# Kernel tuning notes

Measured on AMD Instinct MI355X. Metric: run time of the kernel, lower is better.

Reference implementation:

```python
import jax, jax.numpy as jnp
import numpy as np

N_NODES = 50000
N_EDGES = 800000
IN_FEATS = 128
OUT_CLASSES = 128


def _glorot(key, shape):
    fan_in, fan_out = shape[1], shape[0]
    limit = float(np.sqrt(6.0 / (fan_in + fan_out)))
    return jax.random.uniform(key, shape, jnp.float32, -limit, limit)


def setup_inputs() -> dict:
    key = jax.random.key(0)
    ks = jax.random.split(key, 11)
    x = jax.random.normal(ks[0], (N_NODES, IN_FEATS), jnp.float32)
    edge_index = jax.random.randint(ks[1], (2, N_EDGES), 0, N_NODES, jnp.int64)
    h = OUT_CLASSES // 2
    # PyG SAGEConv: lin_l applied to aggregated neighbors (has bias), lin_r to root (no bias)
    return {
        "x": x,
        "edge_index": edge_index,
        "W_l1": _glorot(ks[2], (OUT_CLASSES, IN_FEATS)),
        "b1": jnp.zeros((OUT_CLASSES,), jnp.float32),
        "W_r1": _glorot(ks[3], (OUT_CLASSES, IN_FEATS)),
        "W_l2": _glorot(ks[4], (h, OUT_CLASSES)),
        "b2": jnp.zeros((h,), jnp.float32),
        "W_r2": _glorot(ks[5], (h, OUT_CLASSES)),
        "W_l3": _glorot(ks[6], (OUT_CLASSES, h)),
        "b3": jnp.zeros((OUT_CLASSES,), jnp.float32),
        "W_r3": _glorot(ks[7], (OUT_CLASSES, h)),
    }


def _sage_conv(x, src, dst, W_l, b, W_r):
    # gather source-node features, mean-aggregate at destinations
    msgs = x[src]                                               # [E, d]
    agg = jax.ops.segment_sum(msgs, dst, num_segments=N_NODES)  # [N, d]
    cnt = jax.ops.segment_sum(jnp.ones((src.shape[0], 1), x.dtype), dst,
                              num_segments=N_NODES)             # [N, 1]
    mean = agg / jnp.maximum(cnt, 1.0)
    return mean @ W_l.T + b + x @ W_r.T


def reference(x, edge_index, W_l1, b1, W_r1, W_l2, b2, W_r2, W_l3, b3, W_r3):
    src, dst = edge_index[0], edge_index[1]
    h = _sage_conv(x, src, dst, W_l1, b1, W_r1)
    h = _sage_conv(h, src, dst, W_l2, b2, W_r2)
    h = _sage_conv(h, src, dst, W_l3, b3, W_r3)
    return h
```

## Files before the change

### kernel.cpp

```cpp
#include <hip/hip_runtime.h>

#define N_NODES 50000
#define N_EDGES 800000
#define BUCKETS 196
#define ECHUNK 4096
#define EBLKS 196
#define BCAP 5120

typedef __attribute__((ext_vector_type(8))) _Float16 half8;
typedef __attribute__((ext_vector_type(4))) float f32x4;


template <int L, int DEPTH>
__device__ __forceinline__ void gather_sum(const half8* __restrict__ ip,
                                           const unsigned short* __restrict__ csr,
                                           int start, int d, int lane,
                                           float acc[8]) {
  if (d <= 0) return;
  int nb = (d + DEPTH - 1) / DEPTH;
  int sc[DEPTH];
#pragma unroll
  for (int j = 0; j < DEPTH; ++j) sc[j] = csr[start + (j < d ? j : d - 1)];
  half8 vlast;
  for (int b = 0; b < nb; ++b) {
    half8 v[DEPTH];
#pragma unroll
    for (int j = 0; j < DEPTH; ++j) v[j] = ip[(size_t)sc[j] * L + lane];
    int e2 = (b + 1) * DEPTH;
    if (e2 < d) {
#pragma unroll
      for (int j = 0; j < DEPTH; ++j) {
        int idx = e2 + j;
        sc[j] = csr[start + (idx < d ? idx : d - 1)];
      }
    }
#pragma unroll
    for (int j = 0; j < DEPTH; ++j)
#pragma unroll
      for (int q = 0; q < 8; ++q) acc[q] += (float)v[j][q];
    vlast = v[DEPTH - 1];
  }
  int rem = d - (nb - 1) * DEPTH;
  if (rem < DEPTH) {
    float corr = (float)(DEPTH - rem);
#pragma unroll
    for (int q = 0; q < 8; ++q) acc[q] -= corr * (float)vlast[q];
  }
}


__global__ __launch_bounds__(256) void prep_k(
    const int* __restrict__ src, const int* __restrict__ dst,
    int* __restrict__ gcur, unsigned* __restrict__ binned,
    const float* __restrict__ x, _Float16* __restrict__ xh,
    const float* __restrict__ Wl1, const float* __restrict__ Wr1,
    const float* __restrict__ Wl2, const float* __restrict__ Wr2,
    const float* __restrict__ Wl3, const float* __restrict__ Wr3,
    _Float16* ph_l1, _Float16* pl_l1, _Float16* ph_r1, _Float16* pl_r1,
    _Float16* ph_c2, _Float16* pl_c2, _Float16* ph_l3, _Float16* pl_l3,
    _Float16* ph_r3, _Float16* pl_r3) {
  int blk = blockIdx.x;
  int t = threadIdx.x;
  if (blk < EBLKS) {
    __shared__ int h[BUCKETS];
    __shared__ int base[BUCKETS];
    for (int i = t; i < BUCKETS; i += 256) h[i] = 0;
    __syncthreads();
    int e0 = blk * ECHUNK;
    int eend = e0 + ECHUNK < N_EDGES ? e0 + ECHUNK : N_EDGES;
    for (int e = e0 + t; e < eend; e += 256) atomicAdd(&h[dst[e] >> 8], 1);
    __syncthreads();
    for (int i = t; i < BUCKETS; i += 256) {
      if (h[i]) base[i] = atomicAdd(&gcur[i], h[i]);
      h[i] = 0;
    }
    __syncthreads();
    for (int e = e0 + t; e < eend; e += 256) {
      int d = dst[e];
      int b = d >> 8;
      int r = atomicAdd(&h[b], 1);
      binned[(size_t)b * BCAP + base[b] + r] =
          (unsigned)src[e] | ((unsigned)(d & 255) << 16);
    }
  } else if (blk < EBLKS + 32) {
    int g = (blk - EBLKS) * 256 + t;
    const float *S0, *S1 = nullptr;
    _Float16 *ph, *pl;
    int f, K;
    if (g < 2048)      { f = g;        ph = ph_l1; pl = pl_l1; S0 = Wl1; K = 128; }
    else if (g < 4096) { f = g - 2048; ph = ph_r1; pl = pl_r1; S0 = Wr1; K = 128; }
    else if (g < 6144) { f = g - 4096; ph = ph_c2; pl = pl_c2; S0 = Wl2; S1 = Wr2; K = 128; }
    else if (g < 7168) { f = g - 6144; ph = ph_l3; pl = pl_l3; S0 = Wl3; K = 64; }
    else               { f = g - 7168; ph = ph_r3; pl = pl_r3; S0 = Wr3; K = 64; }
    int kb = f >> 9;
    int rem = f & 511;
    int n = rem >> 2;
    int lq = rem & 3;
    const float* srow =
        (S1 && n >= 64) ? (S1 + (size_t)(n - 64) * K) : (S0 + (size_t)n * K);
    int kbase = kb * 32 + lq * 8;
#pragma unroll
    for (int j = 0; j < 8; ++j) {
      float v = srow[kbase + j];
      _Float16 hi = (_Float16)v;
      ph[f * 8 + j] = hi;
      pl[f * 8 + j] = (_Float16)(v - (float)hi);
    }
  } else {
    int i = (blk - EBLKS - 32) * 256 + t;
    if (i >= N_NODES * 16) return;
    const float4* xp = (const float4*)x;
    float4 a = xp[2 * i];
    float4 b = xp[2 * i + 1];
    half8 hh;
    hh[0] = (_Float16)a.x; hh[1] = (_Float16)a.y; hh[2] = (_Float16)a.z; hh[3] = (_Float16)a.w;
    hh[4] = (_Float16)b.x; hh[5] = (_Float16)b.y; hh[6] = (_Float16)b.z; hh[7] = (_Float16)b.w;
    ((half8*)xh)[i] = hh;
  }
}

__global__ __launch_bounds__(256) void bucket_fill_k(const unsigned* __restrict__ binned,
                                                     const int* __restrict__ gcnt,
                                                     int* __restrict__ offs,
                                                     int* __restrict__ deg,
                                                     unsigned short* __restrict__ csr) {
  __shared__ int cnt[256];
  __shared__ int loc[256];
  __shared__ int cur[256];
  int b = blockIdx.x;
  int t = threadIdx.x;
  int base = b * BCAP;
  int end = base + gcnt[b];
  cnt[t] = 0;
  __syncthreads();
  for (int e = base + t; e < end; e += 256) atomicAdd(&cnt[(binned[e] >> 16) & 255], 1);
  __syncthreads();
  loc[t] = cnt[t];
  __syncthreads();
  for (int o = 1; o < 256; o <<= 1) {
    int v = (t >= o) ? loc[t - o] : 0;
    __syncthreads();
    loc[t] += v;
    __syncthreads();
  }
  int excl = loc[t] - cnt[t];
  int node = b * 256 + t;
  if (node < N_NODES) {
    offs[node] = base + excl;
    deg[node] = cnt[t];
  }
  cur[t] = excl;
  __syncthreads();
  for (int e = base + t; e < end; e += 256) {
    unsigned r = binned[e];
    int dl = (r >> 16) & 255;
    int p = atomicAdd(&cur[dl], 1);
    csr[base + p] = (unsigned short)(r & 0xFFFF);
  }
}


template <int D, bool FUSE>
__global__ __launch_bounds__(256, 4) void agg_f16_k(const _Float16* __restrict__ in,
                                                    _Float16* __restrict__ out,
                                                    const int* __restrict__ offs,
                                                    const int* __restrict__ deg,
                                                    const unsigned short* __restrict__ csr,
                                                    const float* __restrict__ bias,
                                                    const _Float16* __restrict__ addend) {
  constexpr int L = D / 8;
  constexpr int NPB = 256 / L;
  int node = blockIdx.x * NPB + threadIdx.x / L;
  int lane = threadIdx.x & (L - 1);
  if (node >= N_NODES) return;
  int start = offs[node];
  int d = deg[node];
  const half8* ip = (const half8*)in;
  float acc[8];
#pragma unroll
  for (int j = 0; j < 8; ++j) acc[j] = 0.f;
  gather_sum<L, 16>(ip, csr, start, d, lane, acc);
  float inv = d > 0 ? 1.0f / (float)d : 0.0f;
  half8 o;
  if constexpr (FUSE) {
    half8 av = ((const half8*)addend)[(size_t)node * L + lane];
#pragma unroll
    for (int q = 0; q < 8; ++q)
      o[q] = (_Float16)(acc[q] * inv + bias[lane * 8 + q] + (float)av[q]);
  } else {
#pragma unroll
    for (int q = 0; q < 8; ++q) o[q] = (_Float16)(acc[q] * inv);
  }
  ((half8*)out)[(size_t)node * L + lane] = o;
}


template <int K, int NB, bool OUT32>
__global__ __launch_bounds__(256, 4) void fused_agg_gemm_k(
    const _Float16* __restrict__ feat,
    const int* __restrict__ offs, const int* __restrict__ deg,
    const unsigned short* __restrict__ csr,
    const _Float16* __restrict__ Wlh, const _Float16* __restrict__ Wll,
    const _Float16* __restrict__ Wrh, const _Float16* __restrict__ Wrl,
    const float* __restrict__ bias, _Float16* __restrict__ C16,
    float* __restrict__ C32) {
  constexpr int L = K / 8;
  static_assert(256 / L == NB, "one lane-group per node");
  constexpr int STRIDE = K + 8;
  constexpr int KB = K / 32;
  constexpr int ROWG = NB / 16;
  constexpr int WPR = 4 / ROWG;
  constexpr int CT = 8 / WPR;
  __shared__ _Float16 Asm[NB * STRIDE];
  int t = threadIdx.x;
  int base = blockIdx.x * NB;
  const half8* ip = (const half8*)feat;
  {
    int lane = t & (L - 1);
    int slot = t / L;
    int node = base + slot;
    float acc[8];
#pragma unroll
    for (int j = 0; j < 8; ++j) acc[j] = 0.f;
    float inv = 0.f;
    if (node < N_NODES) {
      int start = offs[node];
      int d = deg[node];
      gather_sum<L, 16>(ip, csr, start, d, lane, acc);
      inv = d > 0 ? 1.0f / (float)d : 0.0f;
    }
    half8 o;
#pragma unroll
    for (int q = 0; q < 8; ++q) o[q] = (_Float16)(acc[q] * inv);
    *(half8*)&Asm[slot * STRIDE + lane * 8] = o;
  }
  __syncthreads();
  int wave = t >> 6;
  int lane = t & 63;
  int l15 = lane & 15;
  int lq = lane >> 4;
  int rowg = wave / WPR;
  int colbase = (wave % WPR) * (CT * 16);
  int row0 = base + rowg * 16;
  const int woff = (l15 * 4 + lq) * 8;
  f32x4 acc[CT];
#pragma unroll
  for (int c = 0; c < CT; ++c) acc[c] = (f32x4){0.f, 0.f, 0.f, 0.f};
  {
    const _Float16* asrc = &Asm[(rowg * 16 + l15) * STRIDE + lq * 8];
    half8 af[KB];
#pragma unroll
    for (int kb = 0; kb < KB; ++kb) af[kb] = *(const half8*)(asrc + kb * 32);
#pragma unroll
    for (int kb = 0; kb < KB; ++kb) {
#pragma unroll
      for (int ct = 0; ct < CT; ++ct) {
        size_t bi = (size_t)(kb * 128 + colbase + ct * 16) * 32 + woff;
        half8 bh = *(const half8*)(Wlh + bi);
        half8 bl = *(const half8*)(Wll + bi);
        acc[ct] = __builtin_amdgcn_mfma_f32_16x16x32_f16(af[kb], bh, acc[ct], 0, 0, 0);
        acc[ct] = __builtin_amdgcn_mfma_f32_16x16x32_f16(af[kb], bl, acc[ct], 0, 0, 0);
      }
    }
  }
  {
    int arow = row0 + l15;
    if (arow >= N_NODES) arow = N_NODES - 1;
    const _Float16* ab = feat + (size_t)arow * K + lq * 8;
    half8 af[KB];
#pragma unroll
    for (int kb = 0; kb < KB; ++kb) af[kb] = *(const half8*)(ab + kb * 32);
#pragma unroll
    for (int kb = 0; kb < KB; ++kb) {
#pragma unroll
      for (int ct = 0; ct < CT; ++ct) {
        size_t bi = (size_t)(kb * 128 + colbase + ct * 16) * 32 + woff;
        half8 bh = *(const half8*)(Wrh + bi);
        half8 bl = *(const half8*)(Wrl + bi);
        acc[ct] = __builtin_amdgcn_mfma_f32_16x16x32_f16(af[kb], bh, acc[ct], 0, 0, 0);
        acc[ct] = __builtin_amdgcn_mfma_f32_16x16x32_f16(af[kb], bl, acc[ct], 0, 0, 0);
      }
    }
  }
#pragma unroll
  for (int r = 0; r < 4; ++r) {
    int row = row0 + lq * 4 + r;
    if (row >= N_NODES) continue;
#pragma unroll
    for (int ct = 0; ct < CT; ++ct) {
      int col = colbase + ct * 16 + l15;
      float v = acc[ct][r] + bias[col];
      if constexpr (OUT32)
        C32[(size_t)row * 128 + col] = v;
      else
        C16[(size_t)row * 128 + col] = (_Float16)v;
    }
  }
}


template <int K, bool DUAL, bool SPLIT, bool OUT32>
__global__ __launch_bounds__(256, 2) void gemm_f16_k(
    const _Float16* __restrict__ A1, const _Float16* __restrict__ W1h,
    const _Float16* __restrict__ W1l,
    const _Float16* __restrict__ A2, const _Float16* __restrict__ W2h,
    const _Float16* __restrict__ W2l,
    const float* __restrict__ bias, _Float16* __restrict__ C16,
    float* __restrict__ C32, _Float16* __restrict__ O2) {
  int wave = threadIdx.x >> 6;
  int lane = threadIdx.x & 63;
  int l15 = lane & 15;
  int lq = lane >> 4;
  int rowblk = blockIdx.x >> 1;
  int colg = blockIdx.x & 1;
  int rg = rowblk * 4 + wave;
  if (rg >= N_NODES / 16) return;
  int row0 = rg << 4;
  constexpr int KB = K / 32;
  constexpr int NN = 128;
  const int woff = (l15 * 4 + lq) * 8;
  f32x4 acc[4];
#pragma unroll
  for (int c = 0; c < 4; ++c) acc[c] = (f32x4){0.f, 0.f, 0.f, 0.f};
  constexpr int NOP = DUAL ? 2 : 1;
#pragma unroll
  for (int op = 0; op < NOP; ++op) {
    const _Float16* A = op ? A2 : A1;
    const _Float16* Wh = op ? W2h : W1h;
    const _Float16* Wl = op ? W2l : W1l;
    const _Float16* ab = A + (size_t)(row0 + l15) * K + lq * 8;
    half8 af[KB];
#pragma unroll
    for (int kb = 0; kb < KB; ++kb) af[kb] = *(const half8*)(ab + kb * 32);
#pragma unroll
    for (int kb = 0; kb < KB; ++kb) {
#pragma unroll
      for (int ct = 0; ct < 4; ++ct) {
        int n0 = colg * 64 + ct * 16;
        size_t base = (size_t)(kb * NN + n0) * 32 + woff;
        half8 bh = *(const half8*)(Wh + base);
        half8 bl = *(const half8*)(Wl + base);
        acc[ct] = __builtin_amdgcn_mfma_f32_16x16x32_f16(af[kb], bh, acc[ct], 0, 0, 0);
        acc[ct] = __builtin_amdgcn_mfma_f32_16x16x32_f16(af[kb], bl, acc[ct], 0, 0, 0);
      }
    }
  }
#pragma unroll
  for (int r = 0; r < 4; ++r) {
    int row = row0 + lq * 4 + r;
#pragma unroll
    for (int ct = 0; ct < 4; ++ct) {
      int col = colg * 64 + ct * 16 + l15;
      float v = acc[ct][r];
      if constexpr (SPLIT) {
        if (col < 64)
          C16[(size_t)row * 64 + col] = (_Float16)v;
        else
          O2[(size_t)row * 64 + (col - 64)] = (_Float16)v;
      } else {
        v += bias[col];
        if constexpr (OUT32)
          C32[(size_t)row * 128 + col] = v;
        else
          C16[(size_t)row * 128 + col] = (_Float16)v;
      }
    }
  }
}

extern "C" void kernel_launch(void* const* d_in, const int* in_sizes, int n_in,
                              void* d_out, int out_size, void* d_ws, size_t ws_size,
                              hipStream_t stream) {
  const float* x   = (const float*)d_in[0];
  const int* ei    = (const int*)d_in[1];
  const float* Wl1 = (const float*)d_in[2];
  const float* b1  = (const float*)d_in[3];
  const float* Wr1 = (const float*)d_in[4];
  const float* Wl2 = (const float*)d_in[5];
  const float* b2  = (const float*)d_in[6];
  const float* Wr2 = (const float*)d_in[7];
  const float* Wl3 = (const float*)d_in[8];
  const float* b3  = (const float*)d_in[9];
  const float* Wr3 = (const float*)d_in[10];
  float* out = (float*)d_out;

  const int* src = ei;
  const int* dst = ei + N_EDGES;

  char* ws = (char*)d_ws;
  size_t off = 0;
  auto take = [&](size_t bytes) {
    void* p = ws + off;
    off += (bytes + 255) & ~(size_t)255;
    return p;
  };
  int* deg    = (int*)take((size_t)N_NODES * 4);
  int* offs   = (int*)take((size_t)N_NODES * 4);
  int* gcur   = (int*)take((size_t)BUCKETS * 4);
  unsigned* binned = (unsigned*)take((size_t)BUCKETS * BCAP * 4);
  unsigned short* csr = (unsigned short*)take((size_t)BUCKETS * BCAP * 2);
  _Float16* xh  = (_Float16*)take((size_t)N_NODES * 128 * 2);
  _Float16* h1h = (_Float16*)take((size_t)N_NODES * 128 * 2);
  _Float16* Ph  = (_Float16*)take((size_t)N_NODES * 64 * 2);
  _Float16* Rh  = (_Float16*)take((size_t)N_NODES * 64 * 2);
  _Float16* h2h = (_Float16*)take((size_t)N_NODES * 64 * 2);
  _Float16* ph_l1 = (_Float16*)take(16384 * 2);
  _Float16* pl_l1 = (_Float16*)take(16384 * 2);
  _Float16* ph_r1 = (_Float16*)take(16384 * 2);
  _Float16* pl_r1 = (_Float16*)take(16384 * 2);
  _Float16* ph_c2 = (_Float16*)take(16384 * 2);
  _Float16* pl_c2 = (_Float16*)take(16384 * 2);
  _Float16* ph_l3 = (_Float16*)take(8192 * 2);
  _Float16* pl_l3 = (_Float16*)take(8192 * 2);
  _Float16* ph_r3 = (_Float16*)take(8192 * 2);
  _Float16* pl_r3 = (_Float16*)take(8192 * 2);

  hipMemsetAsync(gcur, 0, (size_t)BUCKETS * 4, stream);

  prep_k<<<EBLKS + 32 + 3125, 256, 0, stream>>>(
      src, dst, gcur, binned, x, xh, Wl1, Wr1, Wl2, Wr2, Wl3, Wr3, ph_l1, pl_l1,
      ph_r1, pl_r1, ph_c2, pl_c2, ph_l3, pl_l3, ph_r3, pl_r3);
  bucket_fill_k<<<BUCKETS, 256, 0, stream>>>(binned, gcur, offs, deg, csr);

  fused_agg_gemm_k<128, 16, false><<<3125, 256, 0, stream>>>(
      xh, offs, deg, csr, ph_l1, pl_l1, ph_r1, pl_r1, b1, h1h, nullptr);

  gemm_f16_k<128, false, true, false><<<1564, 256, 0, stream>>>(
      h1h, ph_c2, pl_c2, nullptr, nullptr, nullptr, nullptr, Ph, nullptr, Rh);
  agg_f16_k<64, true><<<1563, 256, 0, stream>>>(Ph, h2h, offs, deg, csr, b2, Rh);

  fused_agg_gemm_k<64, 32, true><<<1563, 256, 0, stream>>>(
      h2h, offs, deg, csr, ph_l3, pl_l3, ph_r3, pl_r3, b3, nullptr, out);
}
```

Measured before the change: 243.7 us.

## Slice layer-1 features into 32-wide column slabs for cache-friendly gather, split GEMM

Stores x in fp16 as four 32-feature column slices so each layer-1 aggregation block gathers from a 3.2MB slice that fits in cache better. The block index is interleaved across slices so neighbouring blocks cover different slices. The fused agg+GEMM for layer 1 is split into a separate sliced aggregation kernel and a standalone MFMA GEMM kernel reading the mean and sliced x. This adds an extra round trip of the mean features through memory and one more launch, in exchange for better gather locality.

```diff
diff --git a/kernel.cpp b/kernel.cpp
--- a/kernel.cpp
+++ b/kernel.cpp
@@ -8,22 +8,29 @@
 #define BCAP 5120
 
 typedef __attribute__((ext_vector_type(8))) _Float16 half8;
+typedef __attribute__((ext_vector_type(4))) _Float16 half4;
 typedef __attribute__((ext_vector_type(4))) float f32x4;
 
-
-template <int L, int DEPTH>
-__device__ __forceinline__ void gather_sum(const half8* __restrict__ ip,
+template <int E> struct hvec;
+template <> struct hvec<8> { typedef half8 t; };
+template <> struct hvec<4> { typedef half4 t; };
+
+
+template <int L, int E, int DEPTH>
+__device__ __forceinline__ void gather_sum(const _Float16* __restrict__ feat,
                                            const unsigned short* __restrict__ csr,
                                            int start, int d, int lane,
-                                           float acc[8]) {
+                                           float* acc) {
+  using V = typename hvec<E>::t;
+  const V* ip = (const V*)feat;
   if (d <= 0) return;
   int nb = (d + DEPTH - 1) / DEPTH;
   int sc[DEPTH];
 #pragma unroll
   for (int j = 0; j < DEPTH; ++j) sc[j] = csr[start + (j < d ? j : d - 1)];
-  half8 vlast;
+  V vlast;
   for (int b = 0; b < nb; ++b) {
-    half8 v[DEPTH];
+    V v[DEPTH];
 #pragma unroll
     for (int j = 0; j < DEPTH; ++j) v[j] = ip[(size_t)sc[j] * L + lane];
     int e2 = (b + 1) * DEPTH;
@@ -37,14 +44,14 @@
 #pragma unroll
     for (int j = 0; j < DEPTH; ++j)
 #pragma unroll
-      for (int q = 0; q < 8; ++q) acc[q] += (float)v[j][q];
+      for (int q = 0; q < E; ++q) acc[q] += (float)v[j][q];
     vlast = v[DEPTH - 1];
   }
   int rem = d - (nb - 1) * DEPTH;
   if (rem < DEPTH) {
     float corr = (float)(DEPTH - rem);
 #pragma unroll
-    for (int q = 0; q < 8; ++q) acc[q] -= corr * (float)vlast[q];
+    for (int q = 0; q < E; ++q) acc[q] -= corr * (float)vlast[q];
   }
 }
 
@@ -115,7 +122,9 @@
     half8 hh;
     hh[0] = (_Float16)a.x; hh[1] = (_Float16)a.y; hh[2] = (_Float16)a.z; hh[3] = (_Float16)a.w;
     hh[4] = (_Float16)b.x; hh[5] = (_Float16)b.y; hh[6] = (_Float16)b.z; hh[7] = (_Float16)b.w;
-    ((half8*)xh)[i] = hh;
+    int node = i >> 4;
+    int part = i & 15;
+    ((half8*)xh)[(size_t)(part >> 2) * (N_NODES * 4) + (size_t)node * 4 + (part & 3)] = hh;
   }
 }
 
@@ -160,6 +169,97 @@
 }
 
 
+template <int NSL>
+__global__ __launch_bounds__(256, 4) void agg_sliced_k(
+    const _Float16* __restrict__ in_sl, _Float16* __restrict__ out,
+    const int* __restrict__ offs, const int* __restrict__ deg,
+    const unsigned short* __restrict__ csr) {
+  constexpr int COPIES = 8 / NSL;
+  constexpr int F = NSL * 32;
+  int g = blockIdx.x & 7;
+  int s = g % NSL;
+  int chunk = (blockIdx.x >> 3) * COPIES + g / NSL;
+  int t = threadIdx.x;
+  int node = chunk * 32 + (t >> 3);
+  int lane = t & 7;
+  if (node >= N_NODES) return;
+  const _Float16* base = in_sl + (size_t)s * (N_NODES * 32);
+  float acc[4] = {0.f, 0.f, 0.f, 0.f};
+  int start = offs[node];
+  int d = deg[node];
+  gather_sum<8, 4, 16>(base, csr, start, d, lane, acc);
+  float inv = d > 0 ? 1.0f / (float)d : 0.0f;
+  int feat = s * 32 + lane * 4;
+  half4 o;
+#pragma unroll
+  for (int q = 0; q < 4; ++q) o[q] = (_Float16)(acc[q] * inv);
+  *(half4*)(out + (size_t)node * F + feat) = o;
+}
+
+
+__global__ __launch_bounds__(256, 2) void gemm1_k(
+    const _Float16* __restrict__ mh1, const _Float16* __restrict__ xsl,
+    const _Float16* __restrict__ Wlh, const _Float16* __restrict__ Wll,
+    const _Float16* __restrict__ Wrh, const _Float16* __restrict__ Wrl,
+    const float* __restrict__ b1, _Float16* __restrict__ h1) {
+  int wave = threadIdx.x >> 6;
+  int lane = threadIdx.x & 63;
+  int l15 = lane & 15;
+  int lq = lane >> 4;
+  int rowblk = blockIdx.x >> 1;
+  int colg = blockIdx.x & 1;
+  int rg = rowblk * 4 + wave;
+  if (rg >= N_NODES / 16) return;
+  int row0 = rg << 4;
+  const int woff = (l15 * 4 + lq) * 8;
+  f32x4 acc[4];
+#pragma unroll
+  for (int c = 0; c < 4; ++c) acc[c] = (f32x4){0.f, 0.f, 0.f, 0.f};
+  {
+    const _Float16* ab = mh1 + (size_t)(row0 + l15) * 128 + lq * 8;
+    half8 af[4];
+#pragma unroll
+    for (int kb = 0; kb < 4; ++kb) af[kb] = *(const half8*)(ab + kb * 32);
+#pragma unroll
+    for (int kb = 0; kb < 4; ++kb)
+#pragma unroll
+      for (int ct = 0; ct < 4; ++ct) {
+        size_t bi = (size_t)(kb * 128 + colg * 64 + ct * 16) * 32 + woff;
+        half8 bh = *(const half8*)(Wlh + bi);
+        half8 bl = *(const half8*)(Wll + bi);
+        acc[ct] = __builtin_amdgcn_mfma_f32_16x16x32_f16(af[kb], bh, acc[ct], 0, 0, 0);
+        acc[ct] = __builtin_amdgcn_mfma_f32_16x16x32_f16(af[kb], bl, acc[ct], 0, 0, 0);
+      }
+  }
+  {
+    half8 af[4];
+#pragma unroll
+    for (int kb = 0; kb < 4; ++kb)
+      af[kb] = *(const half8*)(xsl + (size_t)kb * (N_NODES * 32) +
+                               (size_t)(row0 + l15) * 32 + lq * 8);
+#pragma unroll
+    for (int kb = 0; kb < 4; ++kb)
+#pragma unroll
+      for (int ct = 0; ct < 4; ++ct) {
+        size_t bi = (size_t)(kb * 128 + colg * 64 + ct * 16) * 32 + woff;
+        half8 bh = *(const half8*)(Wrh + bi);
+        half8 bl = *(const half8*)(Wrl + bi);
+        acc[ct] = __builtin_amdgcn_mfma_f32_16x16x32_f16(af[kb], bh, acc[ct], 0, 0, 0);
+        acc[ct] = __builtin_amdgcn_mfma_f32_16x16x32_f16(af[kb], bl, acc[ct], 0, 0, 0);
+      }
+  }
+#pragma unroll
+  for (int r = 0; r < 4; ++r) {
+    int row = row0 + lq * 4 + r;
+#pragma unroll
+    for (int ct = 0; ct < 4; ++ct) {
+      int col = colg * 64 + ct * 16 + l15;
+      h1[(size_t)row * 128 + col] = (_Float16)(acc[ct][r] + b1[col]);
+    }
+  }
+}
+
+
 template <int D, bool FUSE>
 __global__ __launch_bounds__(256, 4) void agg_f16_k(const _Float16* __restrict__ in,
                                                     _Float16* __restrict__ out,
@@ -175,11 +275,10 @@
   if (node >= N_NODES) return;
   int start = offs[node];
   int d = deg[node];
-  const half8* ip = (const half8*)in;
   float acc[8];
 #pragma unroll
   for (int j = 0; j < 8; ++j) acc[j] = 0.f;
-  gather_sum<L, 16>(ip, csr, start, d, lane, acc);
+  gather_sum<L, 8, 16>(in, csr, start, d, lane, acc);
   float inv = d > 0 ? 1.0f / (float)d : 0.0f;
   half8 o;
   if constexpr (FUSE) {
@@ -214,7 +313,6 @@
   __shared__ _Float16 Asm[NB * STRIDE];
   int t = threadIdx.x;
   int base = blockIdx.x * NB;
-  const half8* ip = (const half8*)feat;
   {
     int lane = t & (L - 1);
     int slot = t / L;
@@ -226,7 +324,7 @@
     if (node < N_NODES) {
       int start = offs[node];
       int d = deg[node];
-      gather_sum<L, 16>(ip, csr, start, d, lane, acc);
+      gather_sum<L, 8, 16>(feat, csr, start, d, lane, acc);
       inv = d > 0 ? 1.0f / (float)d : 0.0f;
     }
     half8 o;
@@ -399,11 +497,12 @@
   int* gcur   = (int*)take((size_t)BUCKETS * 4);
   unsigned* binned = (unsigned*)take((size_t)BUCKETS * BCAP * 4);
   unsigned short* csr = (unsigned short*)take((size_t)BUCKETS * BCAP * 2);
-  _Float16* xh  = (_Float16*)take((size_t)N_NODES * 128 * 2);
-  _Float16* h1h = (_Float16*)take((size_t)N_NODES * 128 * 2);
-  _Float16* Ph  = (_Float16*)take((size_t)N_NODES * 64 * 2);
-  _Float16* Rh  = (_Float16*)take((size_t)N_NODES * 64 * 2);
-  _Float16* h2h = (_Float16*)take((size_t)N_NODES * 64 * 2);
+  _Float16* xh   = (_Float16*)take((size_t)N_NODES * 128 * 2);
+  _Float16* mh1  = (_Float16*)take((size_t)N_NODES * 128 * 2);
+  _Float16* h1h  = (_Float16*)take((size_t)N_NODES * 128 * 2);
+  _Float16* Ph   = (_Float16*)take((size_t)N_NODES * 64 * 2);
+  _Float16* Rh   = (_Float16*)take((size_t)N_NODES * 64 * 2);
+  _Float16* h2h  = (_Float16*)take((size_t)N_NODES * 64 * 2);
   _Float16* ph_l1 = (_Float16*)take(16384 * 2);
   _Float16* pl_l1 = (_Float16*)take(16384 * 2);
   _Float16* ph_r1 = (_Float16*)take(16384 * 2);
@@ -422,8 +521,9 @@
       ph_r1, pl_r1, ph_c2, pl_c2, ph_l3, pl_l3, ph_r3, pl_r3);
   bucket_fill_k<<<BUCKETS, 256, 0, stream>>>(binned, gcur, offs, deg, csr);
 
-  fused_agg_gemm_k<128, 16, false><<<3125, 256, 0, stream>>>(
-      xh, offs, deg, csr, ph_l1, pl_l1, ph_r1, pl_r1, b1, h1h, nullptr);
+  agg_sliced_k<4><<<8 * 782, 256, 0, stream>>>(xh, mh1, offs, deg, csr);
+
+  gemm1_k<<<1564, 256, 0, stream>>>(mh1, xh, ph_l1, pl_l1, ph_r1, pl_r1, b1, h1h);
 
   gemm_f16_k<128, false, true, false><<<1564, 256, 0, stream>>>(
       h1h, ph_c2, pl_c2, nullptr, nullptr, nullptr, nullptr, Ph, nullptr, Rh);
```

Result: slower. 256.8 us (+5.4%).

## Build CSR via global degree atomics, block scan, and atomic scatter

Applied to the files above, without the earlier changes.

Replaces the two-pass bucketed binning (shared-memory histograms plus an intermediate binned buffer and per-bucket fill) with a global per-node degree count using atomics, a per-bucket prefix scan, and a direct atomic scatter of source indices into CSR. This removes the intermediate binned array write/read and the extra shared-memory passes, at the cost of 800k global atomics on 50k counters twice and an extra kernel launch. It also generalizes gather_sum over the vector width, though only width 8 is used.

```diff
diff --git a/kernel.cpp b/kernel.cpp
--- a/kernel.cpp
+++ b/kernel.cpp
@@ -8,22 +8,29 @@
 #define BCAP 5120
 
 typedef __attribute__((ext_vector_type(8))) _Float16 half8;
+typedef __attribute__((ext_vector_type(4))) _Float16 half4;
 typedef __attribute__((ext_vector_type(4))) float f32x4;
 
-
-template <int L, int DEPTH>
-__device__ __forceinline__ void gather_sum(const half8* __restrict__ ip,
+template <int E> struct hvec;
+template <> struct hvec<8> { typedef half8 t; };
+template <> struct hvec<4> { typedef half4 t; };
+
+
+template <int L, int E, int DEPTH>
+__device__ __forceinline__ void gather_sum(const _Float16* __restrict__ feat,
                                            const unsigned short* __restrict__ csr,
                                            int start, int d, int lane,
-                                           float acc[8]) {
+                                           float* acc) {
+  using V = typename hvec<E>::t;
+  const V* ip = (const V*)feat;
   if (d <= 0) return;
   int nb = (d + DEPTH - 1) / DEPTH;
   int sc[DEPTH];
 #pragma unroll
   for (int j = 0; j < DEPTH; ++j) sc[j] = csr[start + (j < d ? j : d - 1)];
-  half8 vlast;
+  V vlast;
   for (int b = 0; b < nb; ++b) {
-    half8 v[DEPTH];
+    V v[DEPTH];
 #pragma unroll
     for (int j = 0; j < DEPTH; ++j) v[j] = ip[(size_t)sc[j] * L + lane];
     int e2 = (b + 1) * DEPTH;
@@ -37,21 +44,21 @@
 #pragma unroll
     for (int j = 0; j < DEPTH; ++j)
 #pragma unroll
-      for (int q = 0; q < 8; ++q) acc[q] += (float)v[j][q];
+      for (int q = 0; q < E; ++q) acc[q] += (float)v[j][q];
     vlast = v[DEPTH - 1];
   }
   int rem = d - (nb - 1) * DEPTH;
   if (rem < DEPTH) {
     float corr = (float)(DEPTH - rem);
 #pragma unroll
-    for (int q = 0; q < 8; ++q) acc[q] -= corr * (float)vlast[q];
+    for (int q = 0; q < E; ++q) acc[q] -= corr * (float)vlast[q];
   }
 }
 
 
 __global__ __launch_bounds__(256) void prep_k(
     const int* __restrict__ src, const int* __restrict__ dst,
-    int* __restrict__ gcur, unsigned* __restrict__ binned,
+    int* __restrict__ deg,
     const float* __restrict__ x, _Float16* __restrict__ xh,
     const float* __restrict__ Wl1, const float* __restrict__ Wr1,
     const float* __restrict__ Wl2, const float* __restrict__ Wr2,
@@ -62,26 +69,9 @@
   int blk = blockIdx.x;
   int t = threadIdx.x;
   if (blk < EBLKS) {
-    __shared__ int h[BUCKETS];
-    __shared__ int base[BUCKETS];
-    for (int i = t; i < BUCKETS; i += 256) h[i] = 0;
-    __syncthreads();
     int e0 = blk * ECHUNK;
     int eend = e0 + ECHUNK < N_EDGES ? e0 + ECHUNK : N_EDGES;
-    for (int e = e0 + t; e < eend; e += 256) atomicAdd(&h[dst[e] >> 8], 1);
-    __syncthreads();
-    for (int i = t; i < BUCKETS; i += 256) {
-      if (h[i]) base[i] = atomicAdd(&gcur[i], h[i]);
-      h[i] = 0;
-    }
-    __syncthreads();
-    for (int e = e0 + t; e < eend; e += 256) {
-      int d = dst[e];
-      int b = d >> 8;
-      int r = atomicAdd(&h[b], 1);
-      binned[(size_t)b * BCAP + base[b] + r] =
-          (unsigned)src[e] | ((unsigned)(d & 255) << 16);
-    }
+    for (int e = e0 + t; e < eend; e += 256) atomicAdd(&deg[dst[e]], 1);
   } else if (blk < EBLKS + 32) {
     int g = (blk - EBLKS) * 256 + t;
     const float *S0, *S1 = nullptr;
@@ -119,23 +109,15 @@
   }
 }
 
-__global__ __launch_bounds__(256) void bucket_fill_k(const unsigned* __restrict__ binned,
-                                                     const int* __restrict__ gcnt,
-                                                     int* __restrict__ offs,
-                                                     int* __restrict__ deg,
-                                                     unsigned short* __restrict__ csr) {
-  __shared__ int cnt[256];
+__global__ __launch_bounds__(256) void scan_k(const int* __restrict__ deg,
+                                              int* __restrict__ offs,
+                                              int* __restrict__ cur) {
   __shared__ int loc[256];
-  __shared__ int cur[256];
   int b = blockIdx.x;
   int t = threadIdx.x;
-  int base = b * BCAP;
-  int end = base + gcnt[b];
-  cnt[t] = 0;
-  __syncthreads();
-  for (int e = base + t; e < end; e += 256) atomicAdd(&cnt[(binned[e] >> 16) & 255], 1);
-  __syncthreads();
-  loc[t] = cnt[t];
+  int node = b * 256 + t;
+  int d = (node < N_NODES) ? deg[node] : 0;
+  loc[t] = d;
   __syncthreads();
   for (int o = 1; o < 256; o <<= 1) {
     int v = (t >= o) ? loc[t - o] : 0;
@@ -143,20 +125,22 @@
     loc[t] += v;
     __syncthreads();
   }
-  int excl = loc[t] - cnt[t];
-  int node = b * 256 + t;
+  int excl = loc[t] - d;
   if (node < N_NODES) {
-    offs[node] = base + excl;
-    deg[node] = cnt[t];
-  }
-  cur[t] = excl;
-  __syncthreads();
-  for (int e = base + t; e < end; e += 256) {
-    unsigned r = binned[e];
-    int dl = (r >> 16) & 255;
-    int p = atomicAdd(&cur[dl], 1);
-    csr[base + p] = (unsigned short)(r & 0xFFFF);
-  }
+    int p = b * BCAP + excl;
+    offs[node] = p;
+    cur[node] = p;
+  }
+}
+
+__global__ __launch_bounds__(256) void scatter_k(const int* __restrict__ src,
+                                                 const int* __restrict__ dst,
+                                                 int* __restrict__ cur,
+                                                 unsigned short* __restrict__ csr) {
+  int e = blockIdx.x * 256 + threadIdx.x;
+  if (e >= N_EDGES) return;
+  int p = atomicAdd(&cur[dst[e]], 1);
+  csr[p] = (unsigned short)src[e];
 }
 
 
@@ -175,11 +159,10 @@
   if (node >= N_NODES) return;
   int start = offs[node];
   int d = deg[node];
-  const half8* ip = (const half8*)in;
   float acc[8];
 #pragma unroll
   for (int j = 0; j < 8; ++j) acc[j] = 0.f;
-  gather_sum<L, 16>(ip, csr, start, d, lane, acc);
+  gather_sum<L, 8, 16>(in, csr, start, d, lane, acc);
   float inv = d > 0 ? 1.0f / (float)d : 0.0f;
   half8 o;
   if constexpr (FUSE) {
@@ -214,7 +197,6 @@
   __shared__ _Float16 Asm[NB * STRIDE];
   int t = threadIdx.x;
   int base = blockIdx.x * NB;
-  const half8* ip = (const half8*)feat;
   {
     int lane = t & (L - 1);
     int slot = t / L;
@@ -226,7 +208,7 @@
     if (node < N_NODES) {
       int start = offs[node];
       int d = deg[node];
-      gather_sum<L, 16>(ip, csr, start, d, lane, acc);
+      gather_sum<L, 8, 16>(feat, csr, start, d, lane, acc);
       inv = d > 0 ? 1.0f / (float)d : 0.0f;
     }
     half8 o;
@@ -396,8 +378,7 @@
   };
   int* deg    = (int*)take((size_t)N_NODES * 4);
   int* offs   = (int*)take((size_t)N_NODES * 4);
-  int* gcur   = (int*)take((size_t)BUCKETS * 4);
-  unsigned* binned = (unsigned*)take((size_t)BUCKETS * BCAP * 4);
+  int* cur    = (int*)take((size_t)N_NODES * 4);
   unsigned short* csr = (unsigned short*)take((size_t)BUCKETS * BCAP * 2);
   _Float16* xh  = (_Float16*)take((size_t)N_NODES * 128 * 2);
   _Float16* h1h = (_Float16*)take((size_t)N_NODES * 128 * 2);
@@ -415,12 +396,13 @@
   _Float16* ph_r3 = (_Float16*)take(8192 * 2);
   _Float16* pl_r3 = (_Float16*)take(8192 * 2);
 
-  hipMemsetAsync(gcur, 0, (size_t)BUCKETS * 4, stream);
+  hipMemsetAsync(deg, 0, (size_t)N_NODES * 4, stream);
 
   prep_k<<<EBLKS + 32 + 3125, 256, 0, stream>>>(
-      src, dst, gcur, binned, x, xh, Wl1, Wr1, Wl2, Wr2, Wl3, Wr3, ph_l1, pl_l1,
+      src, dst, deg, x, xh, Wl1, Wr1, Wl2, Wr2, Wl3, Wr3, ph_l1, pl_l1,
       ph_r1, pl_r1, ph_c2, pl_c2, ph_l3, pl_l3, ph_r3, pl_r3);
-  bucket_fill_k<<<BUCKETS, 256, 0, stream>>>(binned, gcur, offs, deg, csr);
+  scan_k<<<BUCKETS, 256, 0, stream>>>(deg, offs, cur);
+  scatter_k<<<3125, 256, 0, stream>>>(src, dst, cur, csr);
 
   fused_agg_gemm_k<128, 16, false><<<3125, 256, 0, stream>>>(
       xh, offs, deg, csr, ph_l1, pl_l1, ph_r1, pl_r1, b1, h1h, nullptr);
```

New measurement: 291.1 us. 1.19x slower.
